# Performance work log

Measured on AMD Instinct MI355X. Metric: run time of the kernel, lower is better.

Reference implementation:

```python
import jax, jax.numpy as jnp
import numpy as np

R_FACTOR = 5  # reduction factor r from Tacotron.__init__


def _gru(x, h, Wx, Wh, b):
    # standard GRU cell: z,r,candidate gates packed along last dim of Wx/Wh/b
    H = h.shape[-1]
    gx = x @ Wx
    gh = h @ Wh
    z = jax.nn.sigmoid(gx[..., :H] + gh[..., :H] + b[:H])
    r = jax.nn.sigmoid(gx[..., H:2 * H] + gh[..., H:2 * H] + b[H:2 * H])
    c = jnp.tanh(gx[..., 2 * H:] + r * gh[..., 2 * H:] + b[2 * H:])
    return (1.0 - z) * h + z * c


def setup_inputs() -> dict:
    key = jax.random.key(0)
    ks = jax.random.split(key, 16)
    T_out, B, D = 1000, 128, 80     # decoder frames, batch, mel dim
    T_in, H, P = 512, 256, 128      # encoder steps, hidden, prenet out
    n = lambda k, shp, d: jax.random.normal(k, shp, dtype=jnp.float32) * (1.0 / np.sqrt(d))
    return {
        "outputs": jax.random.normal(ks[0], (T_out, B, D), dtype=jnp.float32),
        "memory": jax.random.normal(ks[1], (T_in, B, H), dtype=jnp.float32),
        "W_pre0": n(ks[2], (D, H), D), "b_pre0": jnp.zeros((H,), jnp.float32),
        "W_pre1": n(ks[3], (H, P), H), "b_pre1": jnp.zeros((P,), jnp.float32),
        "Wx_att": n(ks[4], (P, 3 * H), P), "Wh_att": n(ks[5], (H, 3 * H), H), "b_att": jnp.zeros((3 * H,), jnp.float32),
        "Wq": n(ks[6], (H, H), H), "Wm": n(ks[7], (H, H), H), "v_att": n(ks[8], (H,), H),
        "Wx_d0": n(ks[9], (2 * H, 3 * H), 2 * H), "Wh_d0": n(ks[10], (H, 3 * H), H), "b_d0": jnp.zeros((3 * H,), jnp.float32),
        "Wx_d1": n(ks[11], (H, 3 * H), H), "Wh_d1": n(ks[12], (H, 3 * H), H), "b_d1": jnp.zeros((3 * H,), jnp.float32),
        "Wo": n(ks[13], (H, D), H), "bo": jnp.zeros((D,), jnp.float32),
    }


def _forward(outputs, memory, W_pre0, b_pre0, W_pre1, b_pre1, Wx_att, Wh_att, b_att,
             Wq, Wm, v_att, Wx_d0, Wh_d0, b_d0, Wx_d1, Wh_d1, b_d1, Wo, bo):
    r = R_FACTOR
    T_out, B, D = outputs.shape
    H = memory.shape[-1]
    R = T_out // r  # reduced_time_steps
    # teacher-forcing frame per reduced step: indic[t*r + r - 1] with r zero-frames
    # prepended == outputs[t*r - 1] for t>=1, zeros for t=0.
    frames = jnp.concatenate(
        [jnp.zeros((1, B, D), outputs.dtype), outputs[r - 1::r][: R - 1]], axis=0)  # [R,B,D]
    # precompute attention keys once (AttModule over static memory)
    keys = jnp.einsum('tbh,hk->tbk', memory, Wm)  # [T_in,B,H]
    h0 = jnp.zeros((B, H), outputs.dtype)

    def step(state, frame):
        h_att, h_d0, h_d1 = state
        # pre-net (dropout inactive: inference-mode reference)
        pre = jax.nn.relu(frame @ W_pre0 + b_pre0)
        pre = jax.nn.relu(pre @ W_pre1 + b_pre1)
        # attention RNN
        query = _gru(pre, h_att, Wx_att, Wh_att, b_att)  # [B,H]
        # additive attention
        e = jnp.einsum('tbk,k->tb', jnp.tanh(keys + query @ Wq), v_att)  # [T_in,B]
        alpha = jax.nn.softmax(e, axis=0)
        context = jnp.einsum('tb,tbh->bh', alpha, memory)  # [B,H]
        # decoder cell 0 conditioned on context, with residual from query
        out0 = _gru(jnp.concatenate([query, context], axis=-1), h_d0, Wx_d0, Wh_d0, b_d0)
        res0 = query + out0
        # residual-wrapped decoder cell 1
        out1 = _gru(res0, h_d1, Wx_d1, Wh_d1, b_d1)
        res1 = res0 + out1
        dense = res1 @ Wo + bo  # [B,D]
        return (query, out0, out1), (dense, alpha)

    _, (dense_seq, alpha_seq) = jax.lax.scan(step, (h0, h0, h0), frames)
    # each reduced-step output is written to r consecutive output frames
    final_output = jnp.repeat(dense_seq, r, axis=0)  # [T_out,B,D]
    return final_output, alpha_seq  # alpha_seq: [R,B,T_in]... axes (R,T_in,B) -> transpose


def reference(outputs, memory, W_pre0, b_pre0, W_pre1, b_pre1, Wx_att, Wh_att, b_att,
              Wq, Wm, v_att, Wx_d0, Wh_d0, b_d0, Wx_d1, Wh_d1, b_d1, Wo, bo):
    final_output, alpha_seq = _forward(outputs, memory, W_pre0, b_pre0, W_pre1, b_pre1,
                                       Wx_att, Wh_att, b_att, Wq, Wm, v_att,
                                       Wx_d0, Wh_d0, b_d0, Wx_d1, Wh_d1, b_d1, Wo, bo)
    # alpha stacked per reduced step, shape [R, T_in, B] -> [R, B, T_in] as in TF reshape
    final_alpha = jnp.transpose(alpha_seq, (0, 2, 1))
    return final_output, final_alpha
```

## Files before the change

kernel.cpp:

```cpp
#include <hip/hip_runtime.h>

namespace {
constexpr int B = 128;
constexpr int D = 80;
constexpr int H = 256;
constexpr int PP = 128;
constexpr int TIN = 512;
constexpr int RSTEPS = 200;
constexpr int RF = 5;
constexpr int HB = H * B;
}

__device__ __forceinline__ float sigm(float x) { return 1.f / (1.f + __expf(-x)); }
__device__ __forceinline__ float tanh_(float x) { return 1.f - 2.f / (__expf(2.f * x) + 1.f); }
__device__ __forceinline__ unsigned short f2bf(float f) {
  unsigned int u = __float_as_uint(f);
  u += 0x7fffu + ((u >> 16) & 1u);
  return (unsigned short)(u >> 16);
}
__device__ __forceinline__ void bf2x(unsigned int w, float& f0, float& f1) {
  f0 = __uint_as_float(w << 16);
  f1 = __uint_as_float(w & 0xffff0000u);
}
__device__ __forceinline__ void unpack8(uint4 w, float* f) {
  bf2x(w.x, f[0], f[1]); bf2x(w.y, f[2], f[3]);
  bf2x(w.z, f[4], f[5]); bf2x(w.w, f[6], f[7]);
}
__device__ __forceinline__ float dot8(uint4 w, float4 x0, float4 x1) {
  float f0, f1, a;
  bf2x(w.x, f0, f1); a  = f0 * x0.x + f1 * x0.y;
  bf2x(w.y, f0, f1); a += f0 * x0.z + f1 * x0.w;
  bf2x(w.z, f0, f1); a += f0 * x1.x + f1 * x1.y;
  bf2x(w.w, f0, f1); a += f0 * x1.z + f1 * x1.w;
  return a;
}

__global__ __launch_bounds__(256) void k_keys(const float* __restrict__ mem,
                                              const float* __restrict__ Wm,
                                              unsigned short* __restrict__ keysB) {
  const int k = threadIdx.x;
  const int m0 = blockIdx.x * 32;
  const float* xb = mem + (size_t)m0 * H;
  float acc[32];
#pragma unroll
  for (int i = 0; i < 32; ++i) acc[i] = 0.f;
  for (int h = 0; h < H; h += 4) {
    const float w0 = Wm[(h + 0) * H + k];
    const float w1 = Wm[(h + 1) * H + k];
    const float w2 = Wm[(h + 2) * H + k];
    const float w3 = Wm[(h + 3) * H + k];
#pragma unroll
    for (int mi = 0; mi < 32; ++mi) {
      const float4 x = *reinterpret_cast<const float4*>(xb + (size_t)mi * H + h);
      acc[mi] += x.x * w0 + x.y * w1 + x.z * w2 + x.w * w3;
    }
  }
#pragma unroll
  for (int mi = 0; mi < 32; ++mi) {
    const int m = m0 + mi, t = m >> 7, bb = m & 127;
    keysB[((size_t)bb * TIN + t) * H + k] = f2bf(acc[mi]);
  }
}

__global__ __launch_bounds__(256) void k_memB(const float* __restrict__ mem,
                                              unsigned short* __restrict__ memB) {
  const int m = blockIdx.x, t = m >> 7, bb = m & 127;
  memB[((size_t)bb * TIN + t) * H + threadIdx.x] = f2bf(mem[(size_t)m * H + threadIdx.x]);
}

__global__ __launch_bounds__(256) void k_packWq(const float* __restrict__ W,
                                                unsigned short* __restrict__ Wp) {
  const int idx = blockIdx.x * 256 + threadIdx.x;
  const int k = idx >> 8, c = idx & 255;
  Wp[(((size_t)(k >> 3) * 256) + c) * 8 + (k & 7)] = f2bf(W[idx]);
}

__global__ __launch_bounds__(256) void k_packG(const float* __restrict__ W,
                                               unsigned short* __restrict__ dst,
                                               int K, int rowOff) {
  const int idx = blockIdx.x * 256 + threadIdx.x;
  if (idx >= K * 768) return;
  const int k = idx / 768, c = idx - k * 768;
  const int g = c >> 8, j = c & 255;
  dst[((size_t)(rowOff + k) * 128 + (j >> 1)) * 8 + (j & 1) * 4 + g] = f2bf(W[idx]);
}

__global__ __launch_bounds__(256) void k_prenet(
    const float* __restrict__ outs, const float* __restrict__ Wp0,
    const float* __restrict__ bp0, const float* __restrict__ Wp1,
    const float* __restrict__ bp1, float* __restrict__ preT) {
  const int t = blockIdx.x >> 7, b = blockIdx.x & 127, tid = threadIdx.x;
  __shared__ float f[80];
  __shared__ float p0[256];
  __shared__ float s2[256];
  if (tid < 80)
    f[tid] = (t == 0) ? 0.f
                      : __builtin_nontemporal_load(
                            &outs[((size_t)(t * RF - 1) * B + b) * D + tid]);
  __syncthreads();
  {
    float a = bp0[tid];
#pragma unroll 8
    for (int k = 0; k < 80; ++k) a += f[k] * Wp0[k * 256 + tid];
    p0[tid] = fmaxf(a, 0.f);
  }
  __syncthreads();
  {
    const int c = tid & 127, kh = tid >> 7;
    float a = 0.f;
#pragma unroll 8
    for (int k = kh * 128; k < kh * 128 + 128; ++k) a += p0[k] * Wp1[k * 128 + c];
    s2[kh * 128 + c] = a;
  }
  __syncthreads();
  if (tid < 128)
    preT[((size_t)t * PP + tid) * B + b] = fmaxf(bp1[tid] + s2[tid] + s2[128 + tid], 0.f);
}

__device__ void gru_body(const unsigned short* __restrict__ wp, int K1, int K2,
                         int KH, const float* __restrict__ xT1,
                         const float* __restrict__ xT2,
                         const float* __restrict__ hT_old,
                         const float* __restrict__ b3, float* __restrict__ hT_new,
                         const float* __restrict__ resInT,
                         float* __restrict__ resOutT, int rel, float* smem) {
  const int tid = threadIdx.x;
  float* part = smem;
  float* red = smem + 8192;
  const int jg2 = rel >> 1, bh = rel & 1;
  const int lane = tid & 63, wv = tid >> 6;
  const int b = bh * 64 + lane;

  const uint4* wp4 = reinterpret_cast<const uint4*>(wp);
  const int K12 = K1 + K2, KT = K12 + KH;
  const int KS = KT >> 4;
  const int k0 = wv * KS, k1 = k0 + KS;

  float az0 = 0, ar0 = 0, acx0 = 0, ach0 = 0;
  float az1 = 0, ar1 = 0, acx1 = 0, ach1 = 0;
  float f0, f1;

  const int e1 = (k1 < K1) ? k1 : K1;
#pragma unroll 4
  for (int k = k0; k < e1; ++k) {
    const uint4 w = wp4[(size_t)k * 128 + jg2];
    const float x = xT1[k * B + b];
    bf2x(w.x, f0, f1); az0 += f0 * x; ar0 += f1 * x;
    bf2x(w.y, f0, f1); acx0 += f0 * x;
    bf2x(w.z, f0, f1); az1 += f0 * x; ar1 += f1 * x;
    bf2x(w.w, f0, f1); acx1 += f0 * x;
  }
  const int s2 = (k0 > K1) ? k0 : K1, e2 = (k1 < K12) ? k1 : K12;
#pragma unroll 4
  for (int k = s2; k < e2; ++k) {
    const uint4 w = wp4[(size_t)k * 128 + jg2];
    const float x = xT2[(k - K1) * B + b];
    bf2x(w.x, f0, f1); az0 += f0 * x; ar0 += f1 * x;
    bf2x(w.y, f0, f1); acx0 += f0 * x;
    bf2x(w.z, f0, f1); az1 += f0 * x; ar1 += f1 * x;
    bf2x(w.w, f0, f1); acx1 += f0 * x;
  }
  const int s3 = (k0 > K12) ? k0 : K12;
#pragma unroll 4
  for (int k = s3; k < k1; ++k) {
    const uint4 w = wp4[(size_t)k * 128 + jg2];
    const float x = hT_old[(k - K12) * B + b];
    bf2x(w.x, f0, f1); az0 += f0 * x; ar0 += f1 * x;
    bf2x(w.y, f0, f1); ach0 += f0 * x;
    bf2x(w.z, f0, f1); az1 += f0 * x; ar1 += f1 * x;
    bf2x(w.w, f0, f1); ach1 += f0 * x;
  }

  float* pw = part + wv * 512;
  pw[0 * 64 + lane] = az0;  pw[1 * 64 + lane] = ar0;
  pw[2 * 64 + lane] = acx0; pw[3 * 64 + lane] = ach0;
  pw[4 * 64 + lane] = az1;  pw[5 * 64 + lane] = ar1;
  pw[6 * 64 + lane] = acx1; pw[7 * 64 + lane] = ach1;
  __syncthreads();
  if (tid < 512) {
    float s = 0.f;
#pragma unroll
    for (int w = 0; w < 16; ++w) s += part[w * 512 + tid];
    red[tid] = s;
  }
  __syncthreads();
  if (tid < 128) {
    const int jl = tid >> 6, ln = tid & 63;
    const int j = jg2 * 2 + jl;
    const int bb = bh * 64 + ln;
    const float az = red[(jl * 4 + 0) * 64 + ln];
    const float ar = red[(jl * 4 + 1) * 64 + ln];
    const float acx = red[(jl * 4 + 2) * 64 + ln];
    const float ach = red[(jl * 4 + 3) * 64 + ln];
    const float z = sigm(az + b3[j]);
    const float r = sigm(ar + b3[H + j]);
    const float c = tanh_(acx + r * ach + b3[2 * H + j]);
    const float hold = hT_old[j * B + bb];
    const float hn = (1.f - z) * hold + z * c;
    hT_new[j * B + bb] = hn;
    if (resOutT) resOutT[j * B + bb] = resInT[j * B + bb] + hn;
  }
}

__device__ void dense_body(int s, int b, const float* __restrict__ res1T,
                           const float* __restrict__ Wo,
                           const float* __restrict__ bo, float* __restrict__ dout,
                           float* smem) {
  const int tid = threadIdx.x;
  float* red = smem;
  float* part = smem + 512;
  if (tid < 256) red[tid] = res1T[tid * B + b];
  __syncthreads();
  {
    const int ks = tid >> 7, c = tid & 127;
    float a = 0.f;
    if (c < D) {
#pragma unroll 8
      for (int k = ks * 32; k < ks * 32 + 32; ++k) a += red[k] * Wo[k * D + c];
    }
    part[ks * 128 + c] = a;
  }
  __syncthreads();
  if (tid < D) {
    float dv = bo[tid];
#pragma unroll
    for (int ks = 0; ks < 8; ++ks) dv += part[ks * 128 + tid];
    const size_t base = (size_t)s * RF * (B * D) + (size_t)b * D + tid;
#pragma unroll
    for (int i = 0; i < RF; ++i)
      __builtin_nontemporal_store(dv, &dout[base + (size_t)i * (B * D)]);
  }
}

__device__ void attn_body(int t, int b, const float* __restrict__ qT,
                          const unsigned short* __restrict__ wqB,
                          const float* __restrict__ v_att,
                          const unsigned short* __restrict__ keysB,
                          const unsigned short* __restrict__ memB,
                          float* __restrict__ ctxT, float* __restrict__ alpha,
                          float* smem) {
  const int tid = threadIdx.x;
  const int lane = tid & 63, wv = tid >> 6;
  float* hA = smem;
  float* qk_p = smem + 256;
  float* v_p = smem + 544;
  float* scr = smem + 832;
  float* ep = smem + 9024;
  float* r16 = smem + 9536;
  float* bc = smem + 9552;

  if (tid < 256) {
    hA[tid] = qT[tid * B + b];
    v_p[(tid >> 4) * 18 + (tid & 15)] = v_att[tid];
  }
  __syncthreads();
  const float4* hA4 = reinterpret_cast<const float4*>(hA);
  const uint4* wQ = reinterpret_cast<const uint4*>(wqB);

  {
    const int c = tid & 255, ks = tid >> 8;
    float a = 0.f;
#pragma unroll
    for (int q = 0; q < 8; ++q) {
      const int kg = ks * 8 + q;
      a += dot8(wQ[(size_t)kg * 256 + c], hA4[kg * 2], hA4[kg * 2 + 1]);
    }
    scr[ks * 256 + c] = a;
  }
  __syncthreads();
  if (tid < 256)
    qk_p[(tid >> 4) * 18 + (tid & 15)] =
        scr[tid] + scr[256 + tid] + scr[512 + tid] + scr[768 + tid];
  __syncthreads();

  {
    const int l16 = tid & 15, g = tid >> 4;
    float qg[16], vg[16];
#pragma unroll
    for (int i = 0; i < 16; ++i) {
      qg[i] = qk_p[l16 * 18 + i];
      vg[i] = v_p[l16 * 18 + i];
    }
    const uint4* kB = reinterpret_cast<const uint4*>(keysB + (size_t)b * TIN * H);
#pragma unroll
    for (int p = 0; p < 4; ++p) {
      const int t1 = g + p * 128, t2 = t1 + 64;
      const uint4 a0 = kB[(size_t)t1 * 32 + l16 * 2], a1 = kB[(size_t)t1 * 32 + l16 * 2 + 1];
      const uint4 b0 = kB[(size_t)t2 * 32 + l16 * 2], b1 = kB[(size_t)t2 * 32 + l16 * 2 + 1];
      float ka[16], kb2[16];
      unpack8(a0, ka); unpack8(a1, ka + 8);
      unpack8(b0, kb2); unpack8(b1, kb2 + 8);
      float s1 = 0.f, s2 = 0.f;
#pragma unroll
      for (int i = 0; i < 16; ++i) {
        s1 += vg[i] * tanh_(ka[i] + qg[i]);
        s2 += vg[i] * tanh_(kb2[i] + qg[i]);
      }
#pragma unroll
      for (int m = 1; m < 16; m <<= 1) { s1 += __shfl_xor(s1, m, 16); s2 += __shfl_xor(s2, m, 16); }
      if (l16 == 0) { ep[t1] = s1; ep[t2] = s2; }
    }
  }
  __syncthreads();

  float ev = -1e30f, pv = 0.f;
  if (tid < TIN) {
    ev = ep[tid];
    float mx = ev;
#pragma unroll
    for (int m = 1; m < 64; m <<= 1) mx = fmaxf(mx, __shfl_xor(mx, m));
    if (lane == 0) r16[wv] = mx;
  }
  __syncthreads();
  if (tid == 0) {
    float g = r16[0];
#pragma unroll
    for (int w = 1; w < 8; ++w) g = fmaxf(g, r16[w]);
    bc[0] = g;
  }
  __syncthreads();
  const float M = bc[0];
  if (tid < TIN) {
    pv = __expf(ev - M);
    ep[tid] = pv;
    float s = pv;
#pragma unroll
    for (int m = 1; m < 64; m <<= 1) s += __shfl_xor(s, m);
    if (lane == 0) r16[wv] = s;
  }
  __syncthreads();
  if (tid == 0) {
    float s = 0.f;
#pragma unroll
    for (int w = 0; w < 8; ++w) s += r16[w];
    bc[1] = 1.f / s;
  }
  __syncthreads();
  const float inv = bc[1];
  if (tid < TIN)
    __builtin_nontemporal_store(pv * inv, &alpha[((size_t)t * B + b) * TIN + tid]);

  {
    const int kq8 = tid & 31, ts = tid >> 5;
    float a[8] = {0.f, 0.f, 0.f, 0.f, 0.f, 0.f, 0.f, 0.f};
    const uint4* mB = reinterpret_cast<const uint4*>(memB + (size_t)b * TIN * H);
#pragma unroll 4
    for (int i = 0; i < 16; ++i) {
      const int tt = ts * 16 + i;
      const float p = ep[tt];
      float mv[8];
      unpack8(mB[(size_t)tt * 32 + kq8], mv);
#pragma unroll
      for (int j = 0; j < 8; ++j) a[j] += p * mv[j];
    }
    float4* s4 = reinterpret_cast<float4*>(scr + ts * 256 + kq8 * 8);
    s4[0] = make_float4(a[0], a[1], a[2], a[3]);
    s4[1] = make_float4(a[4], a[5], a[6], a[7]);
  }
  __syncthreads();
  if (tid < 256) {
    float s = 0.f;
#pragma unroll
    for (int ts2 = 0; ts2 < 32; ++ts2) s += scr[ts2 * 256 + tid];
    ctxT[tid * B + b] = inv * s;
  }
}

__global__ __launch_bounds__(1024) void k_pipe(
    int i, const unsigned short* __restrict__ wgA,
    const unsigned short* __restrict__ wg0, const unsigned short* __restrict__ wg1,
    const unsigned short* __restrict__ wqB, const float* __restrict__ v_att,
    const float* __restrict__ b_att, const float* __restrict__ b_d0,
    const float* __restrict__ b_d1, const unsigned short* __restrict__ keysB,
    const unsigned short* __restrict__ memB, const float* __restrict__ preT,
    float* __restrict__ qr, float* __restrict__ ctxr, float* __restrict__ hd0r,
    float* __restrict__ hd1r, float* __restrict__ res0r, float* __restrict__ res1r,
    const float* __restrict__ Wo, const float* __restrict__ bo,
    float* __restrict__ dout, float* __restrict__ alpha) {
  __shared__ alignas(16) float smem[9600];
  const int blk = blockIdx.x;
  if (blk < 128) {
    const int t = i - 1;
    if (t >= 0 && t < RSTEPS)
      attn_body(t, blk, qr + (t & 3) * HB, wqB, v_att, keysB, memB,
                ctxr + (t & 3) * HB, alpha, smem);
  } else if (blk < 384) {
    const int t = i;
    if (t < RSTEPS)
      gru_body(wgA, PP, 0, H, preT + (size_t)t * PP * B, nullptr,
               qr + ((t + 3) & 3) * HB, b_att, qr + (t & 3) * HB, nullptr,
               nullptr, blk - 128, smem);
  } else if (blk < 640) {
    const int t = i - 2;
    if (t >= 0 && t < RSTEPS)
      gru_body(wg0, H, H, H, qr + (t & 3) * HB, ctxr + (t & 3) * HB,
               hd0r + ((t + 3) & 3) * HB, b_d0, hd0r + (t & 3) * HB,
               qr + (t & 3) * HB, res0r + (t & 3) * HB, blk - 384, smem);
  } else if (blk < 896) {
    const int t = i - 3;
    if (t >= 0 && t < RSTEPS)
      gru_body(wg1, H, 0, H, res0r + (t & 3) * HB, nullptr,
               hd1r + ((t + 3) & 3) * HB, b_d1, hd1r + (t & 3) * HB,
               res0r + (t & 3) * HB, res1r + (t & 3) * HB, blk - 640, smem);
  } else {
    const int t = i - 4;
    if (t >= 0 && t < RSTEPS)
      dense_body(t, blk - 896, res1r + (t & 3) * HB, Wo, bo, dout, smem);
  }
}

extern "C" void kernel_launch(void* const* d_in, const int* in_sizes, int n_in,
                              void* d_out, int out_size, void* d_ws,
                              size_t ws_size, hipStream_t stream) {
  const float* outs   = (const float*)d_in[0];
  const float* memory = (const float*)d_in[1];
  const float* Wp0    = (const float*)d_in[2];
  const float* bp0    = (const float*)d_in[3];
  const float* Wp1    = (const float*)d_in[4];
  const float* bp1    = (const float*)d_in[5];
  const float* Wx_att = (const float*)d_in[6];
  const float* Wh_att = (const float*)d_in[7];
  const float* b_att  = (const float*)d_in[8];
  const float* Wq     = (const float*)d_in[9];
  const float* Wm     = (const float*)d_in[10];
  const float* v_att  = (const float*)d_in[11];
  const float* Wx_d0  = (const float*)d_in[12];
  const float* Wh_d0  = (const float*)d_in[13];
  const float* b_d0   = (const float*)d_in[14];
  const float* Wx_d1  = (const float*)d_in[15];
  const float* Wh_d1  = (const float*)d_in[16];
  const float* b_d1   = (const float*)d_in[17];
  const float* Wo     = (const float*)d_in[18];
  const float* bo     = (const float*)d_in[19];
  float* dout = (float*)d_out;
  float* wsf  = (float*)d_ws;

  size_t off = 0;
  unsigned short* keysB = (unsigned short*)(wsf + off); off += (size_t)TIN * B * H / 2;
  unsigned short* memB  = (unsigned short*)(wsf + off); off += (size_t)TIN * B * H / 2;
  unsigned short* wqB   = (unsigned short*)(wsf + off); off += (size_t)256 * 256 / 2;
  unsigned short* wgA   = (unsigned short*)(wsf + off); off += (size_t)384 * 1024 / 2;
  unsigned short* wg0   = (unsigned short*)(wsf + off); off += (size_t)768 * 1024 / 2;
  unsigned short* wg1   = (unsigned short*)(wsf + off); off += (size_t)512 * 1024 / 2;
  float* preT  = wsf + off; off += (size_t)RSTEPS * PP * B;
  float* qr    = wsf + off; off += (size_t)4 * HB;
  float* ctxr  = wsf + off; off += (size_t)4 * HB;
  float* hd0r  = wsf + off; off += (size_t)4 * HB;
  float* hd1r  = wsf + off; off += (size_t)4 * HB;
  float* res0r = wsf + off; off += (size_t)4 * HB;
  float* res1r = wsf + off; off += (size_t)4 * HB;

  hipMemsetAsync(qr + 3 * HB, 0, (size_t)HB * sizeof(float), stream);
  hipMemsetAsync(hd0r + 3 * HB, 0, (size_t)HB * sizeof(float), stream);
  hipMemsetAsync(hd1r + 3 * HB, 0, (size_t)HB * sizeof(float), stream);

  k_keys<<<(TIN * B) / 32, 256, 0, stream>>>(memory, Wm, keysB);
  k_memB<<<TIN * B, 256, 0, stream>>>(memory, memB);
  k_prenet<<<RSTEPS * B, 256, 0, stream>>>(outs, Wp0, bp0, Wp1, bp1, preT);
  k_packWq<<<256, 256, 0, stream>>>(Wq, wqB);
  k_packG<<<(128 * 768 + 255) / 256, 256, 0, stream>>>(Wx_att, wgA, 128, 0);
  k_packG<<<(256 * 768 + 255) / 256, 256, 0, stream>>>(Wh_att, wgA, 256, 128);
  k_packG<<<(512 * 768 + 255) / 256, 256, 0, stream>>>(Wx_d0, wg0, 512, 0);
  k_packG<<<(256 * 768 + 255) / 256, 256, 0, stream>>>(Wh_d0, wg0, 256, 512);
  k_packG<<<(256 * 768 + 255) / 256, 256, 0, stream>>>(Wx_d1, wg1, 256, 0);
  k_packG<<<(256 * 768 + 255) / 256, 256, 0, stream>>>(Wh_d1, wg1, 256, 256);

  float* alpha = dout + (size_t)1000 * B * D;

  for (int i = 0; i < RSTEPS + 4; ++i) {
    k_pipe<<<1024, 1024, 0, stream>>>(i, wgA, wg0, wg1, wqB, v_att, b_att,
                                      b_d0, b_d1, keysB, memB, preT, qr, ctxr,
                                      hd0r, hd1r, res0r, res1r, Wo, bo, dout,
                                      alpha);
  }
}
```

Baseline: 8.857 ms.

## Split attention over two half-sequence blocks with deferred softmax merge

```diff
diff --git a/kernel.cpp b/kernel.cpp
--- a/kernel.cpp
+++ b/kernel.cpp
@@ -120,20 +120,32 @@
 __device__ void gru_body(const unsigned short* __restrict__ wp, int K1, int K2,
                          int KH, const float* __restrict__ xT1,
                          const float* __restrict__ xT2,
+                         const float* __restrict__ pctx0,
+                         const float* __restrict__ msp,
                          const float* __restrict__ hT_old,
                          const float* __restrict__ b3, float* __restrict__ hT_new,
                          const float* __restrict__ resInT,
                          float* __restrict__ resOutT, int rel, float* smem) {
   const int tid = threadIdx.x;
   float* part = smem;
-  float* red = smem + 8192;
+  float* red = smem + 4096;
   const int jg2 = rel >> 1, bh = rel & 1;
   const int lane = tid & 63, wv = tid >> 6;
   const int b = bh * 64 + lane;
 
+  float c0 = 0.f, c1 = 0.f;
+  if (pctx0) {
+    const float m0 = msp[b], s0 = msp[B + b];
+    const float m1 = msp[2 * B + b], s1 = msp[3 * B + b];
+    const float M = fmaxf(m0, m1);
+    const float f0 = __expf(m0 - M), f1 = __expf(m1 - M);
+    const float inv = 1.f / (s0 * f0 + s1 * f1);
+    c0 = f0 * inv; c1 = f1 * inv;
+  }
+
   const uint4* wp4 = reinterpret_cast<const uint4*>(wp);
   const int K12 = K1 + K2, KT = K12 + KH;
-  const int KS = KT >> 4;
+  const int KS = KT >> 3;
   const int k0 = wv * KS, k1 = k0 + KS;
 
   float az0 = 0, ar0 = 0, acx0 = 0, ach0 = 0;
@@ -151,10 +163,12 @@
     bf2x(w.w, f0, f1); acx1 += f0 * x;
   }
   const int s2 = (k0 > K1) ? k0 : K1, e2 = (k1 < K12) ? k1 : K12;
-#pragma unroll 4
+#pragma unroll 2
   for (int k = s2; k < e2; ++k) {
+    const int kk = k - K1;
+    const float x = pctx0 ? (c0 * pctx0[kk * B + b] + c1 * pctx0[(256 + kk) * B + b])
+                          : xT2[kk * B + b];
     const uint4 w = wp4[(size_t)k * 128 + jg2];
-    const float x = xT2[(k - K1) * B + b];
     bf2x(w.x, f0, f1); az0 += f0 * x; ar0 += f1 * x;
     bf2x(w.y, f0, f1); acx0 += f0 * x;
     bf2x(w.z, f0, f1); az1 += f0 * x; ar1 += f1 * x;
@@ -177,10 +191,10 @@
   pw[4 * 64 + lane] = az1;  pw[5 * 64 + lane] = ar1;
   pw[6 * 64 + lane] = acx1; pw[7 * 64 + lane] = ach1;
   __syncthreads();
-  if (tid < 512) {
+  {
     float s = 0.f;
 #pragma unroll
-    for (int w = 0; w < 16; ++w) s += part[w * 512 + tid];
+    for (int w = 0; w < 8; ++w) s += part[w * 512 + tid];
     red[tid] = s;
   }
   __syncthreads();
@@ -205,10 +219,12 @@
 __device__ void dense_body(int s, int b, const float* __restrict__ res1T,
                            const float* __restrict__ Wo,
                            const float* __restrict__ bo, float* __restrict__ dout,
-                           float* smem) {
+                           const float* __restrict__ pvalsS,
+                           const float* __restrict__ msS,
+                           float* __restrict__ alpha, float* smem) {
   const int tid = threadIdx.x;
   float* red = smem;
-  float* part = smem + 512;
+  float* part = smem + 256;
   if (tid < 256) red[tid] = res1T[tid * B + b];
   __syncthreads();
   {
@@ -216,7 +232,7 @@
     float a = 0.f;
     if (c < D) {
 #pragma unroll 8
-      for (int k = ks * 32; k < ks * 32 + 32; ++k) a += red[k] * Wo[k * D + c];
+      for (int k = ks * 64; k < ks * 64 + 64; ++k) a += red[k] * Wo[k * D + c];
     }
     part[ks * 128 + c] = a;
   }
@@ -224,30 +240,38 @@
   if (tid < D) {
     float dv = bo[tid];
 #pragma unroll
-    for (int ks = 0; ks < 8; ++ks) dv += part[ks * 128 + tid];
+    for (int ks = 0; ks < 4; ++ks) dv += part[ks * 128 + tid];
     const size_t base = (size_t)s * RF * (B * D) + (size_t)b * D + tid;
 #pragma unroll
     for (int i = 0; i < RF; ++i)
       __builtin_nontemporal_store(dv, &dout[base + (size_t)i * (B * D)]);
   }
-}
-
-__device__ void attn_body(int t, int b, const float* __restrict__ qT,
-                          const unsigned short* __restrict__ wqB,
-                          const float* __restrict__ v_att,
-                          const unsigned short* __restrict__ keysB,
-                          const unsigned short* __restrict__ memB,
-                          float* __restrict__ ctxT, float* __restrict__ alpha,
-                          float* smem) {
+  const float m0 = msS[b], s0 = msS[B + b], m1 = msS[2 * B + b], s1 = msS[3 * B + b];
+  const float M = fmaxf(m0, m1);
+  const float f0 = __expf(m0 - M), f1 = __expf(m1 - M);
+  const float inv = 1.f / (s0 * f0 + s1 * f1);
+  const float cc = (tid < 256) ? f0 * inv : f1 * inv;
+  __builtin_nontemporal_store(pvalsS[(size_t)b * TIN + tid] * cc,
+                              &alpha[((size_t)s * B + b) * TIN + tid]);
+}
+
+__device__ void attn_half_body(int b, int half, const float* __restrict__ qT,
+                               const unsigned short* __restrict__ wqB,
+                               const float* __restrict__ v_att,
+                               const unsigned short* __restrict__ keysB,
+                               const unsigned short* __restrict__ memB,
+                               float* __restrict__ pvalsS, float* __restrict__ pctxS,
+                               float* __restrict__ msS, float* smem) {
   const int tid = threadIdx.x;
   const int lane = tid & 63, wv = tid >> 6;
+  const int t0 = half * 256;
   float* hA = smem;
   float* qk_p = smem + 256;
   float* v_p = smem + 544;
   float* scr = smem + 832;
-  float* ep = smem + 9024;
-  float* r16 = smem + 9536;
-  float* bc = smem + 9552;
+  float* ep = smem + 4928;
+  float* r16 = smem + 5184;
+  float* bc = smem + 5200;
 
   if (tid < 256) {
     hA[tid] = qT[tid * B + b];
@@ -261,16 +285,15 @@
     const int c = tid & 255, ks = tid >> 8;
     float a = 0.f;
 #pragma unroll
-    for (int q = 0; q < 8; ++q) {
-      const int kg = ks * 8 + q;
+    for (int q = 0; q < 16; ++q) {
+      const int kg = ks * 16 + q;
       a += dot8(wQ[(size_t)kg * 256 + c], hA4[kg * 2], hA4[kg * 2 + 1]);
     }
     scr[ks * 256 + c] = a;
   }
   __syncthreads();
   if (tid < 256)
-    qk_p[(tid >> 4) * 18 + (tid & 15)] =
-        scr[tid] + scr[256 + tid] + scr[512 + tid] + scr[768 + tid];
+    qk_p[(tid >> 4) * 18 + (tid & 15)] = scr[tid] + scr[256 + tid];
   __syncthreads();
 
   {
@@ -284,9 +307,11 @@
     const uint4* kB = reinterpret_cast<const uint4*>(keysB + (size_t)b * TIN * H);
 #pragma unroll
     for (int p = 0; p < 4; ++p) {
-      const int t1 = g + p * 128, t2 = t1 + 64;
-      const uint4 a0 = kB[(size_t)t1 * 32 + l16 * 2], a1 = kB[(size_t)t1 * 32 + l16 * 2 + 1];
-      const uint4 b0 = kB[(size_t)t2 * 32 + l16 * 2], b1 = kB[(size_t)t2 * 32 + l16 * 2 + 1];
+      const int r1 = g + p * 64, r2 = r1 + 32;
+      const uint4 a0 = kB[(size_t)(t0 + r1) * 32 + l16 * 2];
+      const uint4 a1 = kB[(size_t)(t0 + r1) * 32 + l16 * 2 + 1];
+      const uint4 b0 = kB[(size_t)(t0 + r2) * 32 + l16 * 2];
+      const uint4 b1 = kB[(size_t)(t0 + r2) * 32 + l16 * 2 + 1];
       float ka[16], kb2[16];
       unpack8(a0, ka); unpack8(a1, ka + 8);
       unpack8(b0, kb2); unpack8(b1, kb2 + 8);
@@ -298,13 +323,13 @@
       }
 #pragma unroll
       for (int m = 1; m < 16; m <<= 1) { s1 += __shfl_xor(s1, m, 16); s2 += __shfl_xor(s2, m, 16); }
-      if (l16 == 0) { ep[t1] = s1; ep[t2] = s2; }
+      if (l16 == 0) { ep[r1] = s1; ep[r2] = s2; }
     }
   }
   __syncthreads();
 
   float ev = -1e30f, pv = 0.f;
-  if (tid < TIN) {
+  if (tid < 256) {
     ev = ep[tid];
     float mx = ev;
 #pragma unroll
@@ -312,17 +337,14 @@
     if (lane == 0) r16[wv] = mx;
   }
   __syncthreads();
-  if (tid == 0) {
-    float g = r16[0];
-#pragma unroll
-    for (int w = 1; w < 8; ++w) g = fmaxf(g, r16[w]);
-    bc[0] = g;
-  }
+  if (tid == 0)
+    bc[0] = fmaxf(fmaxf(r16[0], r16[1]), fmaxf(r16[2], r16[3]));
   __syncthreads();
   const float M = bc[0];
-  if (tid < TIN) {
+  if (tid < 256) {
     pv = __expf(ev - M);
     ep[tid] = pv;
+    pvalsS[(size_t)b * TIN + t0 + tid] = pv;
     float s = pv;
 #pragma unroll
     for (int m = 1; m < 64; m <<= 1) s += __shfl_xor(s, m);
@@ -330,15 +352,9 @@
   }
   __syncthreads();
   if (tid == 0) {
-    float s = 0.f;
-#pragma unroll
-    for (int w = 0; w < 8; ++w) s += r16[w];
-    bc[1] = 1.f / s;
-  }
-  __syncthreads();
-  const float inv = bc[1];
-  if (tid < TIN)
-    __builtin_nontemporal_store(pv * inv, &alpha[((size_t)t * B + b) * TIN + tid]);
+    msS[half * 2 * B + b] = M;
+    msS[(half * 2 + 1) * B + b] = r16[0] + r16[1] + r16[2] + r16[3];
+  }
 
   {
     const int kq8 = tid & 31, ts = tid >> 5;
@@ -349,7 +365,7 @@
       const int tt = ts * 16 + i;
       const float p = ep[tt];
       float mv[8];
-      unpack8(mB[(size_t)tt * 32 + kq8], mv);
+      unpack8(mB[(size_t)(t0 + tt) * 32 + kq8], mv);
 #pragma unroll
       for (int j = 0; j < 8; ++j) a[j] += p * mv[j];
     }
@@ -361,51 +377,65 @@
   if (tid < 256) {
     float s = 0.f;
 #pragma unroll
-    for (int ts2 = 0; ts2 < 32; ++ts2) s += scr[ts2 * 256 + tid];
-    ctxT[tid * B + b] = inv * s;
-  }
-}
-
-__global__ __launch_bounds__(1024) void k_pipe(
+    for (int ts2 = 0; ts2 < 16; ++ts2) s += scr[ts2 * 256 + tid];
+    pctxS[(size_t)(half * 256 + tid) * B + b] = s;
+  }
+}
+
+__global__ __launch_bounds__(512, 8) void k_pipe(
     int i, const unsigned short* __restrict__ wgA,
     const unsigned short* __restrict__ wg0, const unsigned short* __restrict__ wg1,
     const unsigned short* __restrict__ wqB, const float* __restrict__ v_att,
     const float* __restrict__ b_att, const float* __restrict__ b_d0,
     const float* __restrict__ b_d1, const unsigned short* __restrict__ keysB,
     const unsigned short* __restrict__ memB, const float* __restrict__ preT,
-    float* __restrict__ qr, float* __restrict__ ctxr, float* __restrict__ hd0r,
-    float* __restrict__ hd1r, float* __restrict__ res0r, float* __restrict__ res1r,
+    float* __restrict__ qr, float* __restrict__ hd0r, float* __restrict__ hd1r,
+    float* __restrict__ res0r, float* __restrict__ res1r,
+    float* __restrict__ pvals, float* __restrict__ pctx, float* __restrict__ ms,
     const float* __restrict__ Wo, const float* __restrict__ bo,
     float* __restrict__ dout, float* __restrict__ alpha) {
-  __shared__ alignas(16) float smem[9600];
+  __shared__ alignas(16) float smem[5248];
   const int blk = blockIdx.x;
-  if (blk < 128) {
+  if (blk < 256) {
     const int t = i - 1;
-    if (t >= 0 && t < RSTEPS)
-      attn_body(t, blk, qr + (t & 3) * HB, wqB, v_att, keysB, memB,
-                ctxr + (t & 3) * HB, alpha, smem);
-  } else if (blk < 384) {
+    if (t >= 0 && t < RSTEPS) {
+      const int sl = t & 3;
+      attn_half_body(blk >> 1, blk & 1, qr + (size_t)sl * HB, wqB, v_att, keysB,
+                     memB, pvals + (size_t)sl * B * TIN,
+                     pctx + (size_t)sl * 2 * HB, ms + (size_t)sl * 4 * B, smem);
+    }
+  } else if (blk < 512) {
     const int t = i;
     if (t < RSTEPS)
-      gru_body(wgA, PP, 0, H, preT + (size_t)t * PP * B, nullptr,
-               qr + ((t + 3) & 3) * HB, b_att, qr + (t & 3) * HB, nullptr,
-               nullptr, blk - 128, smem);
-  } else if (blk < 640) {
+      gru_body(wgA, PP, 0, H, preT + (size_t)t * PP * B, nullptr, nullptr,
+               nullptr, qr + (size_t)((t + 3) & 3) * HB, b_att,
+               qr + (size_t)(t & 3) * HB, nullptr, nullptr, blk - 256, smem);
+  } else if (blk < 768) {
     const int t = i - 2;
-    if (t >= 0 && t < RSTEPS)
-      gru_body(wg0, H, H, H, qr + (t & 3) * HB, ctxr + (t & 3) * HB,
-               hd0r + ((t + 3) & 3) * HB, b_d0, hd0r + (t & 3) * HB,
-               qr + (t & 3) * HB, res0r + (t & 3) * HB, blk - 384, smem);
-  } else if (blk < 896) {
+    if (t >= 0 && t < RSTEPS) {
+      const int sl = t & 3;
+      gru_body(wg0, H, H, H, qr + (size_t)sl * HB, nullptr,
+               pctx + (size_t)sl * 2 * HB, ms + (size_t)sl * 4 * B,
+               hd0r + (size_t)((t + 3) & 3) * HB, b_d0,
+               hd0r + (size_t)sl * HB, qr + (size_t)sl * HB,
+               res0r + (size_t)sl * HB, blk - 512, smem);
+    }
+  } else if (blk < 1024) {
     const int t = i - 3;
-    if (t >= 0 && t < RSTEPS)
-      gru_body(wg1, H, 0, H, res0r + (t & 3) * HB, nullptr,
-               hd1r + ((t + 3) & 3) * HB, b_d1, hd1r + (t & 3) * HB,
-               res0r + (t & 3) * HB, res1r + (t & 3) * HB, blk - 640, smem);
+    if (t >= 0 && t < RSTEPS) {
+      const int sl = t & 3;
+      gru_body(wg1, H, 0, H, res0r + (size_t)sl * HB, nullptr, nullptr, nullptr,
+               hd1r + (size_t)((t + 3) & 3) * HB, b_d1, hd1r + (size_t)sl * HB,
+               res0r + (size_t)sl * HB, res1r + (size_t)sl * HB, blk - 768, smem);
+    }
   } else {
     const int t = i - 4;
-    if (t >= 0 && t < RSTEPS)
-      dense_body(t, blk - 896, res1r + (t & 3) * HB, Wo, bo, dout, smem);
+    if (t >= 0 && t < RSTEPS) {
+      const int sl = t & 3;
+      dense_body(t, blk - 1024, res1r + (size_t)sl * HB, Wo, bo, dout,
+                 pvals + (size_t)sl * B * TIN, ms + (size_t)sl * 4 * B, alpha,
+                 smem);
+    }
   }
 }
 
@@ -444,11 +474,13 @@
   unsigned short* wg1   = (unsigned short*)(wsf + off); off += (size_t)512 * 1024 / 2;
   float* preT  = wsf + off; off += (size_t)RSTEPS * PP * B;
   float* qr    = wsf + off; off += (size_t)4 * HB;
-  float* ctxr  = wsf + off; off += (size_t)4 * HB;
   float* hd0r  = wsf + off; off += (size_t)4 * HB;
   float* hd1r  = wsf + off; off += (size_t)4 * HB;
   float* res0r = wsf + off; off += (size_t)4 * HB;
   float* res1r = wsf + off; off += (size_t)4 * HB;
+  float* pvals = wsf + off; off += (size_t)4 * B * TIN;
+  float* pctx  = wsf + off; off += (size_t)4 * 2 * HB;
+  float* ms    = wsf + off; off += (size_t)4 * 4 * B;
 
   hipMemsetAsync(qr + 3 * HB, 0, (size_t)HB * sizeof(float), stream);
   hipMemsetAsync(hd0r + 3 * HB, 0, (size_t)HB * sizeof(float), stream);
@@ -468,9 +500,9 @@
   float* alpha = dout + (size_t)1000 * B * D;
 
   for (int i = 0; i < RSTEPS + 4; ++i) {
-    k_pipe<<<1024, 1024, 0, stream>>>(i, wgA, wg0, wg1, wqB, v_att, b_att,
-                                      b_d0, b_d1, keysB, memB, preT, qr, ctxr,
-                                      hd0r, hd1r, res0r, res1r, Wo, bo, dout,
-                                      alpha);
-  }
-}
+    k_pipe<<<1152, 512, 0, stream>>>(i, wgA, wg0, wg1, wqB, v_att, b_att,
+                                     b_d0, b_d1, keysB, memB, preT, qr, hd0r,
+                                     hd1r, res0r, res1r, pvals, pctx, ms, Wo,
+                                     bo, dout, alpha);
+  }
+}
```

Measured after the change: 7.792 ms. 1.14x faster.
